# Performance work log

Hardware: AMD Instinct MI355X
Metric: run time of the kernel (lower is better)

## Reference

```python
import jax, jax.numpy as jnp
import numpy as np

B, T, C = 2, 2048, 2048
H, HD = 16, 128          # n_head, head_dim
D_C, D_C1, D_ROPE = 512, 512, 64
D_NOPE = HD - D_ROPE     # 64
M = 4                    # move_slots
EPS = 1.1920929e-07      # torch fp32 rms_norm default eps


def _rope(x, cos, sin):
    # x: (B,T,h,D), cos/sin: (B,T,D//2) -> broadcast over head axis
    c = cos[:, :, None, :]
    s = sin[:, :, None, :]
    x1, x2 = jnp.split(x, 2, axis=-1)
    return jnp.concatenate([x1 * c + x2 * s, -x1 * s + x2 * c], axis=-1)


def _rmsnorm(x):
    return x * jax.lax.rsqrt(jnp.mean(x * x, axis=-1, keepdims=True) + EPS)


def setup_inputs() -> dict:
    key = jax.random.key(0)
    ks = jax.random.split(key, 8)
    # realistic decoupled-RoPE angles over d_rope//2 frequencies
    inv_freq = 1.0 / (10000.0 ** (np.arange(0, D_ROPE, 2) / D_ROPE))  # (32,)
    ang = np.arange(T)[:, None] * inv_freq[None, :]                   # (T,32)
    cos = jnp.broadcast_to(jnp.cos(ang)[None].astype(jnp.float32), (B, T, D_ROPE // 2))
    sin = jnp.broadcast_to(jnp.sin(ang)[None].astype(jnp.float32), (B, T, D_ROPE // 2))
    return {
        "x": jax.random.normal(ks[0], (B, T, C), jnp.float32),
        "ve": jax.random.normal(ks[1], (B, T, M * H * HD), jnp.float32),
        "cos": cos,
        "sin": sin,
        "w_down": jax.random.normal(ks[2], (C, D_C + D_C1 + D_ROPE), jnp.float32) * 0.02,
        "w_ukv": jax.random.normal(ks[3], (D_C, H * (D_NOPE + HD)), jnp.float32) * 0.02,
        "w_uq": jax.random.normal(ks[4], (D_C1, H * HD), jnp.float32) * 0.02,
        "w_gate": jax.random.normal(ks[5], (C, H * (M + 1)), jnp.float32) * 0.02,
        "w_proj": jax.random.normal(ks[6], (H * HD, C), jnp.float32) * 0.02,
        "window_size": 2048,
    }


def reference(x, ve, cos, sin, w_down, w_ukv, w_uq, w_gate, w_proj, window_size):
    # fused down projection, split into kv-latent / q-latent / rope part
    down = x @ w_down                                          # (B,T,1088)
    c_kv, c_q, k_rope_raw = jnp.split(down, [D_C, D_C + D_C1], axis=-1)

    kv = (c_kv @ w_ukv).reshape(B, T, H, D_NOPE + HD)
    k_nope, v = jnp.split(kv, [D_NOPE], axis=-1)               # (B,T,H,64), (B,T,H,128)

    k_rope = _rope(k_rope_raw.reshape(B, T, 1, D_ROPE), cos, sin)  # (B,T,1,64)

    # MoVE gating: per-head gate on v plus mixture over M value-embedding slots
    ve5 = ve.reshape(B, T, M, H, HD)
    gates = 2.0 * jax.nn.sigmoid(x @ w_gate).reshape(B, T, H, M + 1)
    v = gates[..., 0:1] * v + jnp.einsum('bthm,btmhd->bthd', gates[..., 1:], ve5)

    q = (c_q @ w_uq).reshape(B, T, H, HD)
    q_nope, q_rope = jnp.split(q, [D_NOPE], axis=-1)
    q_rope = _rope(q_rope, cos, sin)

    k = jnp.concatenate([k_nope, jnp.broadcast_to(k_rope, (B, T, H, D_ROPE))], axis=-1)
    q = jnp.concatenate([q_nope, q_rope], axis=-1)
    q, k = _rmsnorm(q), _rmsnorm(k)

    # sliding-window causal attention (flash_attn semantics: j<=i and i-j<=window)
    scale = 1.0 / float(np.sqrt(HD))
    scores = jnp.einsum('bthd,bshd->bhts', q, k) * scale       # (B,H,T,T)
    i = jnp.arange(T)[:, None]
    j = jnp.arange(T)[None, :]
    mask = (j <= i) & ((i - j) <= window_size)
    scores = jnp.where(mask, scores, -jnp.inf)
    attn = jax.nn.softmax(scores, axis=-1)
    y = jnp.einsum('bhts,bshd->bthd', attn, v)                 # (B,T,H,HD)

    return y.reshape(B, T, H * HD) @ w_proj                    # (B,T,C)
```

## Files before the change

kernel.cpp:

```cpp
#include <hip/hip_runtime.h>

typedef unsigned short u16;
typedef __bf16 bfv8 __attribute__((ext_vector_type(8)));
typedef float f32x4 __attribute__((ext_vector_type(4)));
typedef u16 u16x8 __attribute__((ext_vector_type(8)));

#define B_      2
#define T_      2048
#define C_      2048
#define H_      16
#define HD_     128
#define NT_     (B_ * T_)
#define DOWN_N  1088
#define DCAT    1168
#define KV_N    3072
#define Q_N     2048
#define EPS_    1.1920929e-07f
#define CEXP    0.12751879524580262f

__device__ __forceinline__ float b2f(u16 u) {
    union { unsigned u; float f; } c; c.u = ((unsigned)u) << 16; return c.f;
}
__device__ __forceinline__ u16 f2b(float f) {
    union { float f; unsigned u; } c; c.f = f;
    return (u16)((c.u + 0x7FFFu + ((c.u >> 16) & 1u)) >> 16);
}
__device__ __forceinline__ float dynload(const void* p, size_t i, int bf) {
    if (bf) return b2f(((const u16*)p)[i]);
    return ((const float*)p)[i];
}

__global__ void detect_kernel(const unsigned* __restrict__ x, int* __restrict__ flag) {
    __shared__ int cnt;
    if (threadIdx.x == 0) cnt = 0;
    __syncthreads();
    int c = 0;
    for (int i = threadIdx.x; i < 4096; i += 256) {
        const unsigned w = x[i];
        const unsigned e = (w >> 7) & 0xFF;
        if (e >= 105 && e <= 140) ++c;
    }
    atomicAdd(&cnt, c);
    __syncthreads();
    if (threadIdx.x == 0) flag[0] = (cnt > 2300) ? 1 : 0;
}

__global__ __launch_bounds__(256) void cast_kernel(
    const void* __restrict__ in, u16* __restrict__ out, int n, const int* __restrict__ flagp)
{
    const int fl = flagp[0];
    const int i0 = (blockIdx.x * 256 + threadIdx.x) * 8;
    if (i0 + 8 > n) return;
    u16x8 o;
    #pragma unroll
    for (int i = 0; i < 8; ++i) o[i] = f2b(dynload(in, (size_t)i0 + i, fl));
    *(u16x8*)(out + i0) = o;
}

__global__ __launch_bounds__(256) void tcast_kernel(
    const void* __restrict__ in, u16* __restrict__ out, int K, int N, const int* __restrict__ flagp)
{
    const int fl = flagp[0];
    __shared__ float sf[32][33];
    const int n0 = blockIdx.x * 32, k0 = blockIdx.y * 32;
    const int tx = threadIdx.x & 31, ty = threadIdx.x >> 5;
    const int cr = (n0 + tx < N) ? (n0 + tx) : (N - 1);
    #pragma unroll
    for (int i = 0; i < 4; ++i)
        sf[ty + 8 * i][tx] = dynload(in, (size_t)(k0 + ty + 8 * i) * N + cr, fl);
    __syncthreads();
    #pragma unroll
    for (int i = 0; i < 4; ++i) {
        const int n = n0 + ty + 8 * i;
        if (n < N) out[(size_t)n * K + k0 + tx] = f2b(sf[tx][ty + 8 * i]);
    }
}

__device__ __forceinline__ void stc(u16* p, float v)  { *p = f2b(v); }
__device__ __forceinline__ void stc(float* p, float v){ *p = v; }

template <typename TC>
__global__ __launch_bounds__(256) void mfma_gemm(
    const u16* __restrict__ A, int lda,
    const u16* __restrict__ BT, int ldb,
    TC* __restrict__ Cm, int ldc,
    int M, int N, int K)
{
    __shared__ u16 As[128][40];
    __shared__ u16 Bs[128][40];
    const int tid = threadIdx.x;
    const int m0 = blockIdx.y * 128, n0 = blockIdx.x * 128;
    const int w = tid >> 6, l = tid & 63;
    const int wm = (w >> 1) * 64, wn = (w & 1) * 64;
    const int lr = l & 15, lq = l >> 4;
    const int sr = tid >> 1, sh = (tid & 1) * 16;

    f32x4 acc[4][4];
    #pragma unroll
    for (int i = 0; i < 4; ++i)
        #pragma unroll
        for (int j = 0; j < 4; ++j) acc[i][j] = (f32x4){0.f, 0.f, 0.f, 0.f};

    const bool bvalid = (n0 + sr) < N;
    const u16* arow = A + (size_t)(m0 + sr) * lda + sh;
    const u16* brow = BT + (size_t)(bvalid ? (n0 + sr) : 0) * ldb + sh;

    for (int k0 = 0; k0 < K; k0 += 32) {
        u16x8 a0 = *(const u16x8*)(arow + k0);
        u16x8 a1 = *(const u16x8*)(arow + k0 + 8);
        u16x8 b0 = {0,0,0,0,0,0,0,0}, b1 = {0,0,0,0,0,0,0,0};
        if (bvalid) { b0 = *(const u16x8*)(brow + k0); b1 = *(const u16x8*)(brow + k0 + 8); }
        *(u16x8*)&As[sr][sh]     = a0;
        *(u16x8*)&As[sr][sh + 8] = a1;
        *(u16x8*)&Bs[sr][sh]     = b0;
        *(u16x8*)&Bs[sr][sh + 8] = b1;
        __syncthreads();
        bfv8 af[4], bf[4];
        #pragma unroll
        for (int mi = 0; mi < 4; ++mi) af[mi] = *(const bfv8*)&As[wm + mi * 16 + lr][lq * 8];
        #pragma unroll
        for (int ni = 0; ni < 4; ++ni) bf[ni] = *(const bfv8*)&Bs[wn + ni * 16 + lr][lq * 8];
        #pragma unroll
        for (int mi = 0; mi < 4; ++mi)
            #pragma unroll
            for (int ni = 0; ni < 4; ++ni)
                acc[mi][ni] = __builtin_amdgcn_mfma_f32_16x16x32_bf16(af[mi], bf[ni], acc[mi][ni], 0, 0, 0);
        __syncthreads();
    }

    #pragma unroll
    for (int mi = 0; mi < 4; ++mi) {
        #pragma unroll
        for (int ni = 0; ni < 4; ++ni) {
            const int col = n0 + wn + ni * 16 + lr;
            if (col < N) {
                #pragma unroll
                for (int r = 0; r < 4; ++r) {
                    const int row = m0 + wm + mi * 16 + lq * 4 + r;
                    stc(&Cm[(size_t)row * ldc + col], acc[mi][ni][r]);
                }
            }
        }
    }
}

__global__ __launch_bounds__(256) void assemble_kernel(
    const u16* __restrict__ down,
    const u16* __restrict__ qraw,
    const u16* __restrict__ kv,
    const void* __restrict__ ve,
    const void* __restrict__ cosg,
    const void* __restrict__ sing,
    u16* __restrict__ qo, u16* __restrict__ ko, u16* __restrict__ vo,
    const int* __restrict__ flagp)
{
    const int fl = flagp[0];
    const int bt = blockIdx.x;
    const int tid = threadIdx.x;
    __shared__ float cs[32], sn[32], kr[64];
    if (tid < 32) {
        cs[tid] = dynload(cosg, (size_t)bt * 32 + tid, fl);
        sn[tid] = dynload(sing, (size_t)bt * 32 + tid, fl);
    }
    __syncthreads();
    if (tid < 64) {
        const u16* rp = down + (size_t)bt * DCAT + 1024;
        const int d = tid;
        if (d < 32) kr[d] = b2f(rp[d]) * cs[d] + b2f(rp[d + 32]) * sn[d];
        else { const int r = d - 32; kr[d] = -b2f(rp[d - 32]) * sn[r] + b2f(rp[d]) * cs[r]; }
    }
    __syncthreads();

    const int h = tid >> 4;
    const int lane = tid & 15;
    const int d0 = lane * 8;

    const u16* qr = qraw + (size_t)bt * Q_N + h * HD_;
    float vq[8];
    float ss = 0.f;
    #pragma unroll
    for (int i = 0; i < 8; ++i) {
        const int d = d0 + i;
        float xv = b2f(qr[d]);
        if (d >= 64) {
            if (d < 96) { const int r = d - 64; xv = xv * cs[r] + b2f(qr[d + 32]) * sn[r]; }
            else        { const int r = d - 96; xv = -b2f(qr[d - 32]) * sn[r] + xv * cs[r]; }
        }
        vq[i] = xv; ss += xv * xv;
    }
    #pragma unroll
    for (int off = 1; off < 16; off <<= 1) ss += __shfl_xor(ss, off);
    float rms = rsqrtf(ss * (1.f / 128.f) + EPS_);
    u16* qop = qo + (size_t)bt * Q_N + h * HD_ + d0;
    #pragma unroll
    for (int i = 0; i < 8; ++i) qop[i] = f2b(vq[i] * rms);

    const u16* kvp = kv + (size_t)bt * KV_N + h * 192;
    float vk[8];
    ss = 0.f;
    #pragma unroll
    for (int i = 0; i < 8; ++i) {
        const int d = d0 + i;
        const float xv = (d < 64) ? b2f(kvp[d]) : kr[d - 64];
        vk[i] = xv; ss += xv * xv;
    }
    #pragma unroll
    for (int off = 1; off < 16; off <<= 1) ss += __shfl_xor(ss, off);
    rms = rsqrtf(ss * (1.f / 128.f) + EPS_);
    u16* kop = ko + (size_t)bt * Q_N + h * HD_ + d0;
    #pragma unroll
    for (int i = 0; i < 8; ++i) kop[i] = f2b(vk[i] * rms);

    float g[5];
    #pragma unroll
    for (int j = 0; j < 5; ++j) {
        const float logit = b2f(down[(size_t)bt * DCAT + 1088 + h * 5 + j]);
        g[j] = 2.f / (1.f + expf(-logit));
    }
    const u16* vp = kvp + 64;
    const size_t vebase = (size_t)bt * 8192 + h * HD_;
    u16* vop = vo + (size_t)bt * Q_N + h * HD_ + d0;
    #pragma unroll
    for (int i = 0; i < 8; ++i) {
        const int d = d0 + i;
        float val = g[0] * b2f(vp[d]);
        #pragma unroll
        for (int m = 0; m < 4; ++m) val += g[1 + m] * dynload(ve, vebase + m * 2048 + d, fl);
        vop[i] = f2b(val);
    }
}

__global__ __launch_bounds__(256) void vtrans_kernel(
    const u16* __restrict__ vn, u16* __restrict__ vt)
{
    __shared__ u16 s[64][72];
    const int t0 = blockIdx.x * 64;
    const int d0 = blockIdx.y * 64;
    const int bh = blockIdx.z;
    const int tid = threadIdx.x;
    {
        const int tt = tid >> 2, seg = tid & 3;
        const u16* p = vn + ((size_t)((bh >> 4) * T_) + t0 + tt) * 2048 + (bh & 15) * 128 + d0 + seg * 16;
        u16x8 v0 = *(const u16x8*)(p);
        u16x8 v1 = *(const u16x8*)(p + 8);
        *(u16x8*)&s[tt][seg * 16]     = v0;
        *(u16x8*)&s[tt][seg * 16 + 8] = v1;
    }
    __syncthreads();
    {
        const int dd = tid >> 2, tseg = tid & 3;
        u16* q = vt + ((size_t)(bh * 128) + d0 + dd) * T_ + t0 + tseg * 16;
        #pragma unroll
        for (int g = 0; g < 2; ++g) {
            u16x8 o;
            #pragma unroll
            for (int i = 0; i < 8; ++i) o[i] = s[tseg * 16 + g * 8 + i][dd];
            *(u16x8*)(q + g * 8) = o;
        }
    }
}

__global__ __launch_bounds__(512) void attn_mfma(
    const u16* __restrict__ qn, const u16* __restrict__ kn,
    const u16* __restrict__ vt, u16* __restrict__ yb,
    const int* __restrict__ wptr)
{
    __shared__ u16 Ks[64][136];
    __shared__ u16 VTs[128][72];
    __shared__ u16 Ps[8][16][72];

    const int m0 = blockIdx.x * 128;
    const int h = blockIdx.y, b = blockIdx.z;
    const int W = wptr[0];
    const int tid = threadIdx.x;
    const int w = tid >> 6, l = tid & 63;
    const int lr = l & 15, lq = l >> 4;
    const int qr0 = m0 + w * 16;

    bfv8 qf[4];
    {
        const u16* qp = qn + ((size_t)(b * T_) + qr0 + lr) * 2048 + h * 128 + lq * 8;
        #pragma unroll
        for (int kk = 0; kk < 4; ++kk) qf[kk] = *(const bfv8*)(qp + kk * 32);
    }

    f32x4 oacc[8];
    #pragma unroll
    for (int i = 0; i < 8; ++i) oacc[i] = (f32x4){0.f, 0.f, 0.f, 0.f};
    float m_r[4] = {-1e30f, -1e30f, -1e30f, -1e30f};
    float l_r[4] = {0.f, 0.f, 0.f, 0.f};

    const int kkey = tid >> 3, kseg = tid & 7;
    const int vd = tid >> 2, vh = tid & 3;

    int ns = m0 - W; if (ns < 0) ns = 0; ns &= ~63;
    const int ne = m0 + 64;

    for (int n0 = ns; n0 <= ne; n0 += 64) {
        {
            const u16* kp = kn + ((size_t)(b * T_) + n0 + kkey) * 2048 + h * 128 + kseg * 16;
            u16x8 t0 = *(const u16x8*)(kp);
            u16x8 t1 = *(const u16x8*)(kp + 8);
            *(u16x8*)&Ks[kkey][kseg * 16]     = t0;
            *(u16x8*)&Ks[kkey][kseg * 16 + 8] = t1;
            const u16* vp = vt + ((size_t)(b * H_ + h) * 128 + vd) * T_ + n0 + vh * 16;
            u16x8 v0 = *(const u16x8*)(vp);
            u16x8 v1 = *(const u16x8*)(vp + 8);
            *(u16x8*)&VTs[vd][vh * 16]     = v0;
            *(u16x8*)&VTs[vd][vh * 16 + 8] = v1;
        }
        __syncthreads();

        const bool active = (n0 <= qr0 + 15) && (n0 + 63 >= qr0 - W);
        if (active) {
            f32x4 s[4];
            #pragma unroll
            for (int f = 0; f < 4; ++f) {
                s[f] = (f32x4){0.f, 0.f, 0.f, 0.f};
                #pragma unroll
                for (int kk = 0; kk < 4; ++kk) {
                    bfv8 kf = *(const bfv8*)&Ks[f * 16 + lr][kk * 32 + lq * 8];
                    s[f] = __builtin_amdgcn_mfma_f32_16x16x32_bf16(qf[kk], kf, s[f], 0, 0, 0);
                }
            }

            if ((n0 + 63 > qr0) || (qr0 + 15 - n0 > W)) {
                #pragma unroll
                for (int f = 0; f < 4; ++f) {
                    const int si = n0 + f * 16 + lr;
                    #pragma unroll
                    for (int r = 0; r < 4; ++r) {
                        const int ti = qr0 + lq * 4 + r;
                        if (si > ti || ti - si > W) s[f][r] = -1e30f;
                    }
                }
            }

            float al_r[4];
            #pragma unroll
            for (int r = 0; r < 4; ++r) {
                float mx = fmaxf(fmaxf(s[0][r], s[1][r]), fmaxf(s[2][r], s[3][r]));
                mx = fmaxf(mx, __shfl_xor(mx, 1));
                mx = fmaxf(mx, __shfl_xor(mx, 2));
                mx = fmaxf(mx, __shfl_xor(mx, 4));
                mx = fmaxf(mx, __shfl_xor(mx, 8));
                const float mnew = fmaxf(m_r[r], mx);
                al_r[r] = exp2f((m_r[r] - mnew) * CEXP);
                float ps = 0.f;
                #pragma unroll
                for (int f = 0; f < 4; ++f) {
                    const float sv = s[f][r];
                    const float pv = (sv <= -0.9e30f) ? 0.f : exp2f((sv - mnew) * CEXP);
                    s[f][r] = pv; ps += pv;
                }
                ps += __shfl_xor(ps, 1);
                ps += __shfl_xor(ps, 2);
                ps += __shfl_xor(ps, 4);
                ps += __shfl_xor(ps, 8);
                l_r[r] = l_r[r] * al_r[r] + ps;
                m_r[r] = mnew;
            }
            #pragma unroll
            for (int od = 0; od < 8; ++od)
                #pragma unroll
                for (int r = 0; r < 4; ++r) oacc[od][r] *= al_r[r];

            #pragma unroll
            for (int f = 0; f < 4; ++f)
                #pragma unroll
                for (int r = 0; r < 4; ++r)
                    Ps[w][lq * 4 + r][f * 16 + lr] = f2b(s[f][r]);

            #pragma unroll
            for (int kk2 = 0; kk2 < 2; ++kk2) {
                bfv8 pf = *(const bfv8*)&Ps[w][lr][kk2 * 32 + lq * 8];
                #pragma unroll
                for (int od = 0; od < 8; ++od) {
                    bfv8 vf = *(const bfv8*)&VTs[od * 16 + lr][kk2 * 32 + lq * 8];
                    oacc[od] = __builtin_amdgcn_mfma_f32_16x16x32_bf16(pf, vf, oacc[od], 0, 0, 0);
                }
            }
        }
        __syncthreads();
    }

    float inv[4];
    #pragma unroll
    for (int r = 0; r < 4; ++r) inv[r] = 1.f / l_r[r];
    #pragma unroll
    for (int od = 0; od < 8; ++od)
        #pragma unroll
        for (int r = 0; r < 4; ++r) {
            const size_t idx = ((size_t)(b * T_) + qr0 + lq * 4 + r) * 2048 + h * 128 + od * 16 + lr;
            yb[idx] = f2b(oacc[od][r] * inv[r]);
        }
}

extern "C" void kernel_launch(void* const* d_in, const int* in_sizes, int n_in,
                              void* d_out, int out_size, void* d_ws, size_t ws_size,
                              hipStream_t stream)
{
    const void* x      = d_in[0];
    const void* ve     = d_in[1];
    const void* cosg   = d_in[2];
    const void* sing   = d_in[3];
    const void* w_down = d_in[4];
    const void* w_ukv  = d_in[5];
    const void* w_uq   = d_in[6];
    const void* w_gate = d_in[7];
    const void* w_proj = d_in[8];
    const int*  wsz    = (const int*)d_in[9];
    float* out = (float*)d_out;

    char* p = (char*)d_ws;
    u16* xbf    = (u16*)p; p += (size_t)NT_ * C_ * 2;
    u16* wcatT  = (u16*)p; p += (size_t)DCAT * C_ * 2;
    u16* wukvT  = (u16*)p; p += (size_t)KV_N * 512 * 2;
    u16* wuqT   = (u16*)p; p += (size_t)Q_N * 512 * 2;
    u16* wpT    = (u16*)p; p += (size_t)C_ * C_ * 2;
    u16* downb  = (u16*)p; p += (size_t)NT_ * DCAT * 2;
    u16* kvb    = (u16*)p; p += (size_t)NT_ * KV_N * 2;
    u16* qraw   = (u16*)p; p += (size_t)NT_ * Q_N * 2;
    u16* kn     = (u16*)p; p += (size_t)NT_ * Q_N * 2;
    u16* vn     = (u16*)p; p += (size_t)NT_ * Q_N * 2;
    int* flag   = (int*)p; p += 256;
    u16* qn  = xbf;
    u16* vtb = qraw;
    u16* ybf = vn;

    dim3 blk(256);
    detect_kernel<<<1, blk, 0, stream>>>((const unsigned*)x, flag);
    cast_kernel<<<dim3(NT_ * C_ / (256 * 8)), blk, 0, stream>>>(x, xbf, NT_ * C_, flag);
    tcast_kernel<<<dim3(DOWN_N / 32, C_ / 32), blk, 0, stream>>>(w_down, wcatT, C_, DOWN_N, flag);
    tcast_kernel<<<dim3(3, C_ / 32), blk, 0, stream>>>(w_gate, wcatT + (size_t)DOWN_N * C_, C_, 80, flag);
    tcast_kernel<<<dim3(KV_N / 32, 512 / 32), blk, 0, stream>>>(w_ukv, wukvT, 512, KV_N, flag);
    tcast_kernel<<<dim3(Q_N / 32, 512 / 32), blk, 0, stream>>>(w_uq, wuqT, 512, Q_N, flag);
    tcast_kernel<<<dim3(C_ / 32, C_ / 32), blk, 0, stream>>>(w_proj, wpT, C_, C_, flag);

    mfma_gemm<u16><<<dim3((DCAT + 127) / 128, NT_ / 128), blk, 0, stream>>>(
        xbf, C_, wcatT, C_, downb, DCAT, NT_, DCAT, C_);
    mfma_gemm<u16><<<dim3(KV_N / 128, NT_ / 128), blk, 0, stream>>>(
        downb, DCAT, wukvT, 512, kvb, KV_N, NT_, KV_N, 512);
    mfma_gemm<u16><<<dim3(Q_N / 128, NT_ / 128), blk, 0, stream>>>(
        downb + 512, DCAT, wuqT, 512, qraw, Q_N, NT_, Q_N, 512);
    assemble_kernel<<<dim3(NT_), blk, 0, stream>>>(
        downb, qraw, kvb, ve, cosg, sing, qn, kn, vn, flag);
    vtrans_kernel<<<dim3(T_ / 64, 2, B_ * H_), blk, 0, stream>>>(vn, vtb);
    attn_mfma<<<dim3(T_ / 128, H_, B_), dim3(512), 0, stream>>>(qn, kn, vtb, ybf, wsz);
    mfma_gemm<float><<<dim3(Q_N / 128, NT_ / 128), blk, 0, stream>>>(
        ybf, Q_N, wpT, C_, out, C_, NT_, C_, Q_N);
}
```

Before: 700.6 us.

## Use direct global-to-LDS loads in GEMM and prefetch K/V tiles in attention

The GEMM now stages A/B tiles with global_load_lds into unpadded shared memory, bypassing registers. To do this without bounds checks, the concatenated down/gate weight is zero-padded to a multiple of 128 rows. The attention kernel register-prefetches the next K/V tile while computing the current one, and reverses block order for the second batch to balance causal work. Removing the LDS padding may bring bank conflicts on MFMA fragment reads, and the padding adds extra weight rows to compute.

```diff
diff --git a/kernel.cpp b/kernel.cpp
--- a/kernel.cpp
+++ b/kernel.cpp
@@ -13,6 +13,7 @@
 #define NT_     (B_ * T_)
 #define DOWN_N  1088
 #define DCAT    1168
+#define DCATP   1280
 #define KV_N    3072
 #define Q_N     2048
 #define EPS_    1.1920929e-07f
@@ -28,6 +29,13 @@
 __device__ __forceinline__ float dynload(const void* p, size_t i, int bf) {
     if (bf) return b2f(((const u16*)p)[i]);
     return ((const float*)p)[i];
+}
+
+__device__ __forceinline__ void gload16(const u16* g, u16* l) {
+    __builtin_amdgcn_global_load_lds(
+        (const __attribute__((address_space(1))) void*)g,
+        (__attribute__((address_space(3))) void*)l,
+        16, 0, 0);
 }
 
 __global__ void detect_kernel(const unsigned* __restrict__ x, int* __restrict__ flag) {
@@ -58,7 +66,8 @@
 }
 
 __global__ __launch_bounds__(256) void tcast_kernel(
-    const void* __restrict__ in, u16* __restrict__ out, int K, int N, const int* __restrict__ flagp)
+    const void* __restrict__ in, u16* __restrict__ out, int K, int N, int Ntot,
+    const int* __restrict__ flagp)
 {
     const int fl = flagp[0];
     __shared__ float sf[32][33];
@@ -72,7 +81,7 @@
     #pragma unroll
     for (int i = 0; i < 4; ++i) {
         const int n = n0 + ty + 8 * i;
-        if (n < N) out[(size_t)n * K + k0 + tx] = f2b(sf[tx][ty + 8 * i]);
+        if (n < Ntot) out[(size_t)n * K + k0 + tx] = (n < N) ? f2b(sf[tx][ty + 8 * i]) : (u16)0;
     }
 }
 
@@ -86,14 +95,13 @@
     TC* __restrict__ Cm, int ldc,
     int M, int N, int K)
 {
-    __shared__ u16 As[128][40];
-    __shared__ u16 Bs[128][40];
+    __shared__ u16 As[128 * 32];
+    __shared__ u16 Bs[128 * 32];
     const int tid = threadIdx.x;
     const int m0 = blockIdx.y * 128, n0 = blockIdx.x * 128;
     const int w = tid >> 6, l = tid & 63;
     const int wm = (w >> 1) * 64, wn = (w & 1) * 64;
     const int lr = l & 15, lq = l >> 4;
-    const int sr = tid >> 1, sh = (tid & 1) * 16;
 
     f32x4 acc[4][4];
     #pragma unroll
@@ -101,25 +109,26 @@
         #pragma unroll
         for (int j = 0; j < 4; ++j) acc[i][j] = (f32x4){0.f, 0.f, 0.f, 0.f};
 
-    const bool bvalid = (n0 + sr) < N;
-    const u16* arow = A + (size_t)(m0 + sr) * lda + sh;
-    const u16* brow = BT + (size_t)(bvalid ? (n0 + sr) : 0) * ldb + sh;
+    const int srow = w * 32 + (l >> 2);
+    const int scol = (l & 3) * 8;
+    const u16* ag = A  + (size_t)(m0 + srow) * lda + scol;
+    const u16* bg = BT + (size_t)(n0 + srow) * ldb + scol;
+    u16* as0 = &As[(w * 32) * 32];
+    u16* as1 = &As[(w * 32 + 16) * 32];
+    u16* bs0 = &Bs[(w * 32) * 32];
+    u16* bs1 = &Bs[(w * 32 + 16) * 32];
 
     for (int k0 = 0; k0 < K; k0 += 32) {
-        u16x8 a0 = *(const u16x8*)(arow + k0);
-        u16x8 a1 = *(const u16x8*)(arow + k0 + 8);
-        u16x8 b0 = {0,0,0,0,0,0,0,0}, b1 = {0,0,0,0,0,0,0,0};
-        if (bvalid) { b0 = *(const u16x8*)(brow + k0); b1 = *(const u16x8*)(brow + k0 + 8); }
-        *(u16x8*)&As[sr][sh]     = a0;
-        *(u16x8*)&As[sr][sh + 8] = a1;
-        *(u16x8*)&Bs[sr][sh]     = b0;
-        *(u16x8*)&Bs[sr][sh + 8] = b1;
+        gload16(ag + k0,            as0);
+        gload16(ag + 16 * lda + k0, as1);
+        gload16(bg + k0,            bs0);
+        gload16(bg + 16 * ldb + k0, bs1);
         __syncthreads();
         bfv8 af[4], bf[4];
         #pragma unroll
-        for (int mi = 0; mi < 4; ++mi) af[mi] = *(const bfv8*)&As[wm + mi * 16 + lr][lq * 8];
-        #pragma unroll
-        for (int ni = 0; ni < 4; ++ni) bf[ni] = *(const bfv8*)&Bs[wn + ni * 16 + lr][lq * 8];
+        for (int mi = 0; mi < 4; ++mi) af[mi] = *(const bfv8*)&As[(wm + mi * 16 + lr) * 32 + lq * 8];
+        #pragma unroll
+        for (int ni = 0; ni < 4; ++ni) bf[ni] = *(const bfv8*)&Bs[(wn + ni * 16 + lr) * 32 + lq * 8];
         #pragma unroll
         for (int mi = 0; mi < 4; ++mi)
             #pragma unroll
@@ -269,8 +278,9 @@
     __shared__ u16 VTs[128][72];
     __shared__ u16 Ps[8][16][72];
 
-    const int m0 = blockIdx.x * 128;
     const int h = blockIdx.y, b = blockIdx.z;
+    const int mb = b ? ((int)gridDim.x - 1 - (int)blockIdx.x) : (int)blockIdx.x;
+    const int m0 = mb * 128;
     const int W = wptr[0];
     const int tid = threadIdx.x;
     const int w = tid >> 6, l = tid & 63;
@@ -296,20 +306,34 @@
     int ns = m0 - W; if (ns < 0) ns = 0; ns &= ~63;
     const int ne = m0 + 64;
 
+    const u16* kbase = kn + ((size_t)(b * T_) + kkey) * 2048 + h * 128 + kseg * 16;
+    const u16* vbase = vt + ((size_t)(b * H_ + h) * 128 + vd) * T_ + vh * 16;
+
+    u16x8 pk0, pk1, pv0, pv1;
+    {
+        const u16* kp = kbase + (size_t)ns * 2048;
+        const u16* vp = vbase + ns;
+        pk0 = *(const u16x8*)(kp);
+        pk1 = *(const u16x8*)(kp + 8);
+        pv0 = *(const u16x8*)(vp);
+        pv1 = *(const u16x8*)(vp + 8);
+    }
+
     for (int n0 = ns; n0 <= ne; n0 += 64) {
-        {
-            const u16* kp = kn + ((size_t)(b * T_) + n0 + kkey) * 2048 + h * 128 + kseg * 16;
-            u16x8 t0 = *(const u16x8*)(kp);
-            u16x8 t1 = *(const u16x8*)(kp + 8);
-            *(u16x8*)&Ks[kkey][kseg * 16]     = t0;
-            *(u16x8*)&Ks[kkey][kseg * 16 + 8] = t1;
-            const u16* vp = vt + ((size_t)(b * H_ + h) * 128 + vd) * T_ + n0 + vh * 16;
-            u16x8 v0 = *(const u16x8*)(vp);
-            u16x8 v1 = *(const u16x8*)(vp + 8);
-            *(u16x8*)&VTs[vd][vh * 16]     = v0;
-            *(u16x8*)&VTs[vd][vh * 16 + 8] = v1;
-        }
+        *(u16x8*)&Ks[kkey][kseg * 16]     = pk0;
+        *(u16x8*)&Ks[kkey][kseg * 16 + 8] = pk1;
+        *(u16x8*)&VTs[vd][vh * 16]        = pv0;
+        *(u16x8*)&VTs[vd][vh * 16 + 8]    = pv1;
         __syncthreads();
+
+        if (n0 < ne) {
+            const u16* kp = kbase + (size_t)(n0 + 64) * 2048;
+            const u16* vp = vbase + (n0 + 64);
+            pk0 = *(const u16x8*)(kp);
+            pk1 = *(const u16x8*)(kp + 8);
+            pv0 = *(const u16x8*)(vp);
+            pv1 = *(const u16x8*)(vp + 8);
+        }
 
         const bool active = (n0 <= qr0 + 15) && (n0 + 63 >= qr0 - W);
         if (active) {
@@ -414,7 +438,7 @@
 
     char* p = (char*)d_ws;
     u16* xbf    = (u16*)p; p += (size_t)NT_ * C_ * 2;
-    u16* wcatT  = (u16*)p; p += (size_t)DCAT * C_ * 2;
+    u16* wcatT  = (u16*)p; p += (size_t)DCATP * C_ * 2;
     u16* wukvT  = (u16*)p; p += (size_t)KV_N * 512 * 2;
     u16* wuqT   = (u16*)p; p += (size_t)Q_N * 512 * 2;
     u16* wpT    = (u16*)p; p += (size_t)C_ * C_ * 2;
@@ -431,13 +455,14 @@
     dim3 blk(256);
     detect_kernel<<<1, blk, 0, stream>>>((const unsigned*)x, flag);
     cast_kernel<<<dim3(NT_ * C_ / (256 * 8)), blk, 0, stream>>>(x, xbf, NT_ * C_, flag);
-    tcast_kernel<<<dim3(DOWN_N / 32, C_ / 32), blk, 0, stream>>>(w_down, wcatT, C_, DOWN_N, flag);
-    tcast_kernel<<<dim3(3, C_ / 32), blk, 0, stream>>>(w_gate, wcatT + (size_t)DOWN_N * C_, C_, 80, flag);
-    tcast_kernel<<<dim3(KV_N / 32, 512 / 32), blk, 0, stream>>>(w_ukv, wukvT, 512, KV_N, flag);
-    tcast_kernel<<<dim3(Q_N / 32, 512 / 32), blk, 0, stream>>>(w_uq, wuqT, 512, Q_N, flag);
-    tcast_kernel<<<dim3(C_ / 32, C_ / 32), blk, 0, stream>>>(w_proj, wpT, C_, C_, flag);
-
-    mfma_gemm<u16><<<dim3((DCAT + 127) / 128, NT_ / 128), blk, 0, stream>>>(
+    tcast_kernel<<<dim3(DOWN_N / 32, C_ / 32), blk, 0, stream>>>(w_down, wcatT, C_, DOWN_N, DOWN_N, flag);
+    tcast_kernel<<<dim3((DCATP - DOWN_N) / 32, C_ / 32), blk, 0, stream>>>(
+        w_gate, wcatT + (size_t)DOWN_N * C_, C_, 80, DCATP - DOWN_N, flag);
+    tcast_kernel<<<dim3(KV_N / 32, 512 / 32), blk, 0, stream>>>(w_ukv, wukvT, 512, KV_N, KV_N, flag);
+    tcast_kernel<<<dim3(Q_N / 32, 512 / 32), blk, 0, stream>>>(w_uq, wuqT, 512, Q_N, Q_N, flag);
+    tcast_kernel<<<dim3(C_ / 32, C_ / 32), blk, 0, stream>>>(w_proj, wpT, C_, C_, C_, flag);
+
+    mfma_gemm<u16><<<dim3(DCATP / 128, NT_ / 128), blk, 0, stream>>>(
         xbf, C_, wcatT, C_, downb, DCAT, NT_, DCAT, C_);
     mfma_gemm<u16><<<dim3(KV_N / 128, NT_ / 128), blk, 0, stream>>>(
         downb, DCAT, wukvT, 512, kvb, KV_N, NT_, KV_N, 512);
```

Result: faster. 675.1 us (-3.6%).
